# Kernel optimization log

Hardware: AMD Instinct MI355X
Metric: run time of the kernel (lower is better)

## Reference

```python
import jax, jax.numpy as jnp
import numpy as np


def _min_dist(pixel_coords, points):
    """pixel_coords: (P,2) float, points: (B,N,2) float -> (B,P) min euclidean distance.
    Uses |p-q|^2 = |p|^2 + |q|^2 - 2 p.q to avoid materializing (B,P,N,2)."""
    p2 = jnp.sum(pixel_coords * pixel_coords, axis=-1)          # (P,)
    q2 = jnp.sum(points * points, axis=-1)                      # (B,N)
    dots = jnp.einsum('pc,bnc->bpn', pixel_coords, points)      # (B,P,N)
    d2 = p2[None, :, None] + q2[:, None, :] - 2.0 * dots        # (B,P,N)
    return jnp.sqrt(jnp.maximum(jnp.min(d2, axis=2), 0.0))      # (B,P)


def binary_mask_given_points(height, width, pos_points, neg_points):
    pos_points = pos_points.astype(jnp.float32)
    neg_points = neg_points.astype(jnp.float32)
    gy, gx = jnp.meshgrid(jnp.arange(height, dtype=jnp.float32),
                          jnp.arange(width, dtype=jnp.float32), indexing='ij')
    pixel_coords = jnp.stack((gy, gx), axis=-1).reshape(-1, 2)  # (H*W, 2)
    min_pos = _min_dist(pixel_coords, pos_points)               # (B, H*W)
    min_neg = _min_dist(pixel_coords, neg_points)               # (B, H*W)
    mask = (min_pos < min_neg).astype(jnp.float32)
    return mask.reshape(pos_points.shape[0], height, width)


def setup_inputs() -> dict:
    key = jax.random.key(0)
    k1, k2, k3 = jax.random.split(key, 3)
    B, H, W, N = 8, 512, 512, 50
    out = jax.random.normal(k1, (B, 1, H, W), dtype=jnp.float32)
    pos_clicks = jax.random.randint(k2, (B, N, 2), 0, 512, dtype=jnp.int32)
    neg_clicks = jax.random.randint(k3, (B, N, 2), 0, 512, dtype=jnp.int32)
    return {"out": out, "pos_clicks": pos_clicks, "neg_clicks": neg_clicks}


def reference(out, pos_clicks, neg_clicks):
    H, W = out.shape[2], out.shape[3]
    pseudo_target = binary_mask_given_points(H, W, pos_clicks, neg_clicks)
    pseudo_target = pseudo_target[:, None, :, :]                # (B,1,H,W)
    # BCEWithLogitsLoss (mean reduction), numerically stable form
    x, z = out, pseudo_target
    loss = jnp.mean(jnp.maximum(x, 0.0) - x * z + jnp.log1p(jnp.exp(-jnp.abs(x))))
    return loss, pseudo_target
```

## Files before the change

### kernel.cpp

```cpp
#include <hip/hip_runtime.h>
#include <math.h>

constexpr int B = 8, H = 512, W = 512, N = 50;
constexpr int TS = 32;
constexpr int TPB = (H / TS) * (W / TS);
constexpr int NBLOCKS = B * TPB;
constexpr int KMAX = 2 * N + 4;
constexpr float INF = 3.0e38f;

__global__ __launch_bounds__(256) void psl_main(
    const float* __restrict__ out,
    const int*   __restrict__ pos,
    const int*   __restrict__ neg,
    float*       __restrict__ dout,
    float*       __restrict__ partials)
{
    __shared__ float4 s_pts[KMAX];
    __shared__ float  s_red[4];
    __shared__ int    s_cnt;

    const int bid = blockIdx.x;
    const int t   = threadIdx.x;
    const int b   = bid >> 8;
    const int ty  = (bid >> 4) & 15;
    const int tx  = bid & 15;

    const int r  = t >> 3;
    const int cc = (t & 7) << 2;
    const int y  = ty * TS + r;
    const int x  = tx * TS + cc;
    const size_t pix = ((size_t)(b * H + y)) * W + x;
    const float4 xv = *(const float4*)(out + pix);

    const float y0f = (float)(ty * TS);
    const float x0f = (float)(tx * TS);

    if (t == 0) s_cnt = 0;
    if (t < KMAX) s_pts[t] = make_float4(0.0f, 0.0f, INF, 0.0f);

    float dmax2 = INF;
    float dmin2 = 0.0f, c0 = 0.0f, c1 = 0.0f, c2 = 0.0f;
    if (t < 2 * N) {
        const int* src = (t < N) ? pos : neg;
        const int  idx = (t < N) ? t : t - N;
        int2 p = ((const int2*)src)[b * N + idx];
        const float fy = (float)p.x, fx = (float)p.y;
        const float tag = (t < N) ? 1.0f : 0.0f;
        const float yhi = y0f + (float)(TS - 1), xhi = x0f + (float)(TS - 1);
        float dy = fmaxf(fmaxf(y0f - fy, fy - yhi), 0.0f);
        float dx = fmaxf(fmaxf(x0f - fx, fx - xhi), 0.0f);
        dmin2 = dy * dy + dx * dx;
        float dyM = fmaxf(fy - y0f, yhi - fy);
        float dxM = fmaxf(fx - x0f, xhi - fx);
        dmax2 = dyM * dyM + dxM * dxM;
        c0 = -4.0f * fx;
        c1 = -4.0f * fy;
        c2 = 2.0f * (fx * fx + fy * fy) + tag;
    }
    float m = dmax2;
    #pragma unroll
    for (int off = 32; off > 0; off >>= 1)
        m = fminf(m, __shfl_down(m, off, 64));
    if ((t & 63) == 0) s_red[t >> 6] = m;
    __syncthreads();
    const float bound = fminf(fminf(s_red[0], s_red[1]),
                              fminf(s_red[2], s_red[3]));
    if (t < 2 * N && dmin2 <= bound) {
        int k = atomicAdd(&s_cnt, 1);
        s_pts[k] = make_float4(c0, c1, c2, 0.0f);
    }
    __syncthreads();
    const int K = (s_cnt + 3) & ~3;

    const float xs[4] = {xv.x, xv.y, xv.z, xv.w};
    float lsum = 0.0f;
    #pragma unroll
    for (int j = 0; j < 4; ++j)
        lsum += fmaxf(xs[j], 0.0f) + __logf(1.0f + __expf(-fabsf(xs[j])));

    const float yf = (float)y;
    const float xf = (float)x;
    float mn[4] = {INF, INF, INF, INF};
    for (int n = 0; n < K; n += 4) {
        #pragma unroll
        for (int j = 0; j < 4; ++j) {
            float4 P = s_pts[n + j];
            float cy = fmaf(P.y, yf, P.z);
            mn[0] = fminf(mn[0], fmaf(P.x, xf,          cy));
            mn[1] = fminf(mn[1], fmaf(P.x, xf + 1.0f,   cy));
            mn[2] = fminf(mn[2], fmaf(P.x, xf + 2.0f,   cy));
            mn[3] = fminf(mn[3], fmaf(P.x, xf + 3.0f,   cy));
        }
    }

    #pragma unroll
    for (int j = 0; j < 4; ++j) {
        int mi = (int)mn[j];
        float z = (float)(mi & 1);
        dout[1 + pix + j] = z;
        lsum -= xs[j] * z;
    }

    #pragma unroll
    for (int off = 32; off > 0; off >>= 1)
        lsum += __shfl_down(lsum, off, 64);
    __syncthreads();
    if ((t & 63) == 0) s_red[t >> 6] = lsum;
    __syncthreads();
    if (t == 0)
        partials[bid] = (s_red[0] + s_red[1]) + (s_red[2] + s_red[3]);
}

__global__ __launch_bounds__(256) void psl_finish(
    const float* __restrict__ partials,
    float*       __restrict__ dout)
{
    __shared__ float s_red[4];
    const int t = threadIdx.x;
    float s = ((partials[t]        + partials[t + 256]) +
               (partials[t + 512]  + partials[t + 768])) +
              ((partials[t + 1024] + partials[t + 1280]) +
               (partials[t + 1536] + partials[t + 1792]));
    #pragma unroll
    for (int off = 32; off > 0; off >>= 1)
        s += __shfl_down(s, off, 64);
    if ((t & 63) == 0) s_red[t >> 6] = s;
    __syncthreads();
    if (t == 0)
        dout[0] = ((s_red[0] + s_red[1]) + (s_red[2] + s_red[3])) *
                  (1.0f / (float)(B * H * W));
}

extern "C" void kernel_launch(void* const* d_in, const int* in_sizes, int n_in,
                              void* d_out, int out_size, void* d_ws, size_t ws_size,
                              hipStream_t stream) {
    const float* out_logits = (const float*)d_in[0];
    const int*   pos        = (const int*)d_in[1];
    const int*   neg        = (const int*)d_in[2];
    float* dout     = (float*)d_out;
    float* partials = (float*)d_ws;

    psl_main<<<NBLOCKS, 256, 0, stream>>>(out_logits, pos, neg, dout, partials);
    psl_finish<<<1, 256, 0, stream>>>(partials, dout);
}
```

Before: 12.77 us.

## Split pos/neg candidate lists with ballot compaction and per-wave partial sums

Replaces the combined, parity-tagged candidate list with separate positive and negative lists, each compacted with a wave ballot instead of shared-memory atomics. The mask becomes a direct comparison of two minima, which removes the float-to-int parity trick. That trick could misclassify when the distance encoding lost precision. Each wave now writes its own partial sum, which drops two block syncs at the end, and the finish kernel sums four times as many partials. The cost is two inner loops, each padded to a multiple of four, so slightly more loop overhead and padding work per pixel.

```diff
diff --git a/kernel.cpp b/kernel.cpp
--- a/kernel.cpp
+++ b/kernel.cpp
@@ -3,9 +3,8 @@
 
 constexpr int B = 8, H = 512, W = 512, N = 50;
 constexpr int TS = 32;
-constexpr int TPB = (H / TS) * (W / TS);
-constexpr int NBLOCKS = B * TPB;
-constexpr int KMAX = 2 * N + 4;
+constexpr int NBLOCKS = B * (H / TS) * (W / TS);
+constexpr int LCAP = 56;
 constexpr float INF = 3.0e38f;
 
 __global__ __launch_bounds__(256) void psl_main(
@@ -15,15 +14,24 @@
     float*       __restrict__ dout,
     float*       __restrict__ partials)
 {
-    __shared__ float4 s_pts[KMAX];
+    __shared__ float4 s_p[LCAP];
+    __shared__ float4 s_n[LCAP];
     __shared__ float  s_red[4];
-    __shared__ int    s_cnt;
+    __shared__ int    s_k[2];
 
-    const int bid = blockIdx.x;
-    const int t   = threadIdx.x;
-    const int b   = bid >> 8;
-    const int ty  = (bid >> 4) & 15;
-    const int tx  = bid & 15;
+    const int bid  = blockIdx.x;
+    const int t    = threadIdx.x;
+    const int b    = bid >> 8;
+    const int ty   = (bid >> 4) & 15;
+    const int tx   = bid & 15;
+    const int wave = t >> 6, lane = t & 63;
+
+    const bool isPt = (wave < 2) && (lane < N);
+    int2 p;
+    if (isPt) {
+        const int* src = (wave == 0) ? pos : neg;
+        p = ((const int2*)src)[b * N + lane];
+    }
 
     const int r  = t >> 3;
     const int cc = (t & 7) << 2;
@@ -32,45 +40,47 @@
     const size_t pix = ((size_t)(b * H + y)) * W + x;
     const float4 xv = *(const float4*)(out + pix);
 
-    const float y0f = (float)(ty * TS);
-    const float x0f = (float)(tx * TS);
+    if (t < LCAP) {
+        s_p[t] = make_float4(0.0f, 0.0f, INF, 0.0f);
+        s_n[t] = make_float4(0.0f, 0.0f, INF, 0.0f);
+    }
 
-    if (t == 0) s_cnt = 0;
-    if (t < KMAX) s_pts[t] = make_float4(0.0f, 0.0f, INF, 0.0f);
-
-    float dmax2 = INF;
-    float dmin2 = 0.0f, c0 = 0.0f, c1 = 0.0f, c2 = 0.0f;
-    if (t < 2 * N) {
-        const int* src = (t < N) ? pos : neg;
-        const int  idx = (t < N) ? t : t - N;
-        int2 p = ((const int2*)src)[b * N + idx];
+    const float y0f = (float)(ty * TS), x0f = (float)(tx * TS);
+    float dmin2 = INF, dmax2 = INF, c0 = 0.0f, c1 = 0.0f, c2 = 0.0f;
+    if (isPt) {
         const float fy = (float)p.x, fx = (float)p.y;
-        const float tag = (t < N) ? 1.0f : 0.0f;
-        const float yhi = y0f + (float)(TS - 1), xhi = x0f + (float)(TS - 1);
+        const float yhi = y0f + 31.0f, xhi = x0f + 31.0f;
         float dy = fmaxf(fmaxf(y0f - fy, fy - yhi), 0.0f);
         float dx = fmaxf(fmaxf(x0f - fx, fx - xhi), 0.0f);
         dmin2 = dy * dy + dx * dx;
         float dyM = fmaxf(fy - y0f, yhi - fy);
         float dxM = fmaxf(fx - x0f, xhi - fx);
         dmax2 = dyM * dyM + dxM * dxM;
-        c0 = -4.0f * fx;
-        c1 = -4.0f * fy;
-        c2 = 2.0f * (fx * fx + fy * fy) + tag;
+        c0 = -2.0f * fx;
+        c1 = -2.0f * fy;
+        c2 = fx * fx + fy * fy;
     }
+
     float m = dmax2;
     #pragma unroll
     for (int off = 32; off > 0; off >>= 1)
         m = fminf(m, __shfl_down(m, off, 64));
-    if ((t & 63) == 0) s_red[t >> 6] = m;
+    if (lane == 0) s_red[wave] = m;
     __syncthreads();
     const float bound = fminf(fminf(s_red[0], s_red[1]),
                               fminf(s_red[2], s_red[3]));
-    if (t < 2 * N && dmin2 <= bound) {
-        int k = atomicAdd(&s_cnt, 1);
-        s_pts[k] = make_float4(c0, c1, c2, 0.0f);
+
+    const bool surv = isPt && (dmin2 <= bound);
+    const unsigned long long bal = __ballot(surv);
+    if (surv) {
+        int k = __popcll(bal & ((1ull << lane) - 1ull));
+        if (wave == 0) s_p[k] = make_float4(c0, c1, c2, 0.0f);
+        else           s_n[k] = make_float4(c0, c1, c2, 0.0f);
     }
+    if (wave < 2 && lane == 0) s_k[wave] = (int)__popcll(bal);
     __syncthreads();
-    const int K = (s_cnt + 3) & ~3;
+    const int K0 = (s_k[0] + 3) & ~3;
+    const int K1 = (s_k[1] + 3) & ~3;
 
     const float xs[4] = {xv.x, xv.y, xv.z, xv.w};
     float lsum = 0.0f;
@@ -78,25 +88,35 @@
     for (int j = 0; j < 4; ++j)
         lsum += fmaxf(xs[j], 0.0f) + __logf(1.0f + __expf(-fabsf(xs[j])));
 
-    const float yf = (float)y;
-    const float xf = (float)x;
-    float mn[4] = {INF, INF, INF, INF};
-    for (int n = 0; n < K; n += 4) {
+    const float yf = (float)y, xf = (float)x;
+    float mp[4] = {INF, INF, INF, INF};
+    float mq[4] = {INF, INF, INF, INF};
+    for (int n = 0; n < K0; n += 4) {
         #pragma unroll
         for (int j = 0; j < 4; ++j) {
-            float4 P = s_pts[n + j];
+            float4 P = s_p[n + j];
             float cy = fmaf(P.y, yf, P.z);
-            mn[0] = fminf(mn[0], fmaf(P.x, xf,          cy));
-            mn[1] = fminf(mn[1], fmaf(P.x, xf + 1.0f,   cy));
-            mn[2] = fminf(mn[2], fmaf(P.x, xf + 2.0f,   cy));
-            mn[3] = fminf(mn[3], fmaf(P.x, xf + 3.0f,   cy));
+            mp[0] = fminf(mp[0], fmaf(P.x, xf,        cy));
+            mp[1] = fminf(mp[1], fmaf(P.x, xf + 1.0f, cy));
+            mp[2] = fminf(mp[2], fmaf(P.x, xf + 2.0f, cy));
+            mp[3] = fminf(mp[3], fmaf(P.x, xf + 3.0f, cy));
+        }
+    }
+    for (int n = 0; n < K1; n += 4) {
+        #pragma unroll
+        for (int j = 0; j < 4; ++j) {
+            float4 Q = s_n[n + j];
+            float cy = fmaf(Q.y, yf, Q.z);
+            mq[0] = fminf(mq[0], fmaf(Q.x, xf,        cy));
+            mq[1] = fminf(mq[1], fmaf(Q.x, xf + 1.0f, cy));
+            mq[2] = fminf(mq[2], fmaf(Q.x, xf + 2.0f, cy));
+            mq[3] = fminf(mq[3], fmaf(Q.x, xf + 3.0f, cy));
         }
     }
 
     #pragma unroll
     for (int j = 0; j < 4; ++j) {
-        int mi = (int)mn[j];
-        float z = (float)(mi & 1);
+        float z = (mp[j] < mq[j]) ? 1.0f : 0.0f;
         dout[1 + pix + j] = z;
         lsum -= xs[j] * z;
     }
@@ -104,11 +124,7 @@
     #pragma unroll
     for (int off = 32; off > 0; off >>= 1)
         lsum += __shfl_down(lsum, off, 64);
-    __syncthreads();
-    if ((t & 63) == 0) s_red[t >> 6] = lsum;
-    __syncthreads();
-    if (t == 0)
-        partials[bid] = (s_red[0] + s_red[1]) + (s_red[2] + s_red[3]);
+    if (lane == 0) partials[(bid << 2) + wave] = lsum;
 }
 
 __global__ __launch_bounds__(256) void psl_finish(
@@ -117,10 +133,10 @@
 {
     __shared__ float s_red[4];
     const int t = threadIdx.x;
-    float s = ((partials[t]        + partials[t + 256]) +
-               (partials[t + 512]  + partials[t + 768])) +
-              ((partials[t + 1024] + partials[t + 1280]) +
-               (partials[t + 1536] + partials[t + 1792]));
+    float s = 0.0f;
+    #pragma unroll
+    for (int i = 0; i < 32; ++i)
+        s += partials[t + (i << 8)];
     #pragma unroll
     for (int off = 32; off > 0; off >>= 1)
         s += __shfl_down(s, off, 64);
```

After: 13.39 us. +4.9%, slower.
